# Performance work log

Hardware: AMD Instinct MI355X
Metric: run time of the kernel (lower is better)

Reference implementation:

```python
import jax, jax.numpy as jnp
import numpy as np

B, T, N, D, H = 8, 128, 64, 1024, 512

def setup_inputs() -> dict:
    key = jax.random.key(0)
    ks = jax.random.split(key, 8)
    s = 1.0 / np.sqrt(D)
    return {
        "img_features": jax.random.normal(ks[0], (B, T, N, D), dtype=jnp.float32),
        "hidden_state": jax.random.normal(ks[1], (N, B, D), dtype=jnp.float32),
        "W_weight": jax.random.normal(ks[2], (H, D), dtype=jnp.float32) * s,
        "W_bias": jax.random.normal(ks[3], (H,), dtype=jnp.float32) * s,
        "U_weight": jax.random.normal(ks[4], (H, D), dtype=jnp.float32) * s,
        "U_bias": jax.random.normal(ks[5], (H,), dtype=jnp.float32) * s,
        "w_weight": jax.random.normal(ks[6], (1, H), dtype=jnp.float32) * (1.0 / np.sqrt(H)),
        "w_bias": jax.random.normal(ks[7], (1,), dtype=jnp.float32) * (1.0 / np.sqrt(H)),
    }

def reference(img_features, hidden_state, W_weight, W_bias, U_weight, U_bias, w_weight, w_bias):
    # W_e: [B,T,N,H]
    W_e = jnp.einsum('btnd,hd->btnh', img_features, W_weight) + W_bias
    # U(hidden): [N,B,H]; torch unsqueeze(0).permute(2,0,1,3) -> [B,1,N,H]
    U_h = jnp.einsum('nbd,hd->nbh', hidden_state, U_weight) + U_bias
    U_e = jnp.transpose(U_h, (1, 0, 2))[:, None, :, :]  # [B,1,N,H]
    att = jnp.tanh(W_e + U_e)                            # [B,T,N,H]
    e = jnp.einsum('btnh,h->btn', att, w_weight[0]) + w_bias[0]  # [B,T,N]
    alpha = jax.nn.softmax(e, axis=-1)                   # softmax over objects N
    phi = jnp.einsum('btnd,btn->btd', img_features, alpha)  # [B,T,D]
    return phi
```

## Files before the change

kernel.cpp:

```cpp
#include <hip/hip_runtime.h>
#include <stdint.h>

#define B_ 8
#define T_ 128
#define N_ 64
#define D_ 1024
#define H_ 512

typedef __attribute__((ext_vector_type(8))) short bf16x8;
typedef __attribute__((ext_vector_type(4))) float f32x4;

__device__ __forceinline__ unsigned short f2bf(float x) {
  union { float f; unsigned u; } c; c.f = x;
  unsigned r = c.u + 0x7FFFu + ((c.u >> 16) & 1u);
  return (unsigned short)(r >> 16);
}

__global__ __launch_bounds__(256) void k_transU(const float* __restrict__ U,
                                                float* __restrict__ Ut) {
  __shared__ float tile[32][33];
  int d0 = blockIdx.x * 32, h0 = blockIdx.y * 32;
  int lx = threadIdx.x & 31, ly = threadIdx.x >> 5;
#pragma unroll
  for (int i = 0; i < 32; i += 8)
    tile[ly + i][lx] = U[(size_t)(h0 + ly + i) * D_ + d0 + lx];
  __syncthreads();
#pragma unroll
  for (int i = 0; i < 32; i += 8)
    Ut[(size_t)(d0 + ly + i) * H_ + h0 + lx] = tile[lx][ly + i];
}

__global__ __launch_bounds__(512) void k_convW(const float* __restrict__ W,
                                               unsigned short* __restrict__ Wt) {
  int i = blockIdx.x * 512 + threadIdx.x;
  int e = i & 7, cs = (i >> 3) & 3, h = (i >> 5) & 511, kt = i >> 14;
  int k = kt * 32 + (((cs ^ (h & 3)) << 3) | e);
  Wt[i] = f2bf(W[(size_t)h * D_ + k]);
}

__global__ __launch_bounds__(512) void k_uh(const float* __restrict__ hidden,
                                            const float* __restrict__ Ut,
                                            const float* __restrict__ Ub,
                                            const float* __restrict__ Wb,
                                            float* __restrict__ Uhb) {
  __shared__ float xs[8][1024];
  int b = blockIdx.x >> 3, ng = blockIdx.x & 7, tid = threadIdx.x;
  for (int i = tid; i < 8192; i += 512) {
    int nn = i >> 10, d = i & 1023;
    xs[nn][d] = hidden[(size_t)((ng * 8 + nn) * B_ + b) * D_ + d];
  }
  __syncthreads();
  float acc[8];
#pragma unroll
  for (int nn = 0; nn < 8; ++nn) acc[nn] = 0.f;
  for (int d = 0; d < 1024; ++d) {
    float u = Ut[(size_t)d * H_ + tid];
#pragma unroll
    for (int nn = 0; nn < 8; ++nn) acc[nn] += xs[nn][d] * u;
  }
  float bias = Ub[tid] + Wb[tid];
#pragma unroll
  for (int nn = 0; nn < 8; ++nn)
    Uhb[(size_t)(b * 64 + ng * 8 + nn) * H_ + tid] = acc[nn] + bias;
}

__global__ __launch_bounds__(512, 2) void k_main(const float* __restrict__ img,
                                                 const unsigned short* __restrict__ Wt,
                                                 const float* __restrict__ Uhb,
                                                 const float* __restrict__ ww,
                                                 const float* __restrict__ wb,
                                                 float* __restrict__ alpha) {
  __shared__ __align__(16) unsigned char sA[4096];
  __shared__ __align__(16) unsigned char sB[32768];
  __shared__ float e_part[256];
  const int tid = threadIdx.x;
  const int bt = blockIdx.x;
  const int b = bt >> 7;
  const int lane = tid & 63, w = tid >> 6, wm = w >> 2, wn = w & 3;
  const int lo = lane & 15, hi = lane >> 4;

  const int rowA = tid >> 3, c4 = tid & 7;
  const float* gA = img + (size_t)bt * 65536 + rowA * 1024 + c4 * 4;
  const int sAoff = rowA * 64 + ((((c4 >> 1) ^ (rowA & 3)) << 4) | ((c4 & 1) << 3));
  const uint4* gB = (const uint4*)Wt;

  const int swz = ((hi ^ (lane & 3)) << 4);
  const int base_a = (wm * 32 + lo) * 64 + swz;
  const int base_b = (wn * 128 + lo) * 64 + swz;

  f32x4 acc[2][8] = {};

  for (int kt = 0; kt < 32; ++kt) {
    float4 av = *(const float4*)(gA + kt * 32);
    uint4 b0 = gB[kt * 2048 + 0 * 512 + tid];
    uint4 b1 = gB[kt * 2048 + 1 * 512 + tid];
    uint4 b2 = gB[kt * 2048 + 2 * 512 + tid];
    uint4 b3 = gB[kt * 2048 + 3 * 512 + tid];
    uint2 pk;
    pk.x = (unsigned)f2bf(av.x) | ((unsigned)f2bf(av.y) << 16);
    pk.y = (unsigned)f2bf(av.z) | ((unsigned)f2bf(av.w) << 16);
    *(uint2*)(sA + sAoff) = pk;
    *(uint4*)(sB + (0 * 512 + tid) * 16) = b0;
    *(uint4*)(sB + (1 * 512 + tid) * 16) = b1;
    *(uint4*)(sB + (2 * 512 + tid) * 16) = b2;
    *(uint4*)(sB + (3 * 512 + tid) * 16) = b3;
    __syncthreads();

    bf16x8 aF0 = *(const bf16x8*)(sA + base_a);
    bf16x8 aF1 = *(const bf16x8*)(sA + base_a + 1024);
    bf16x8 bF[8];
#pragma unroll
    for (int nf = 0; nf < 8; ++nf) bF[nf] = *(const bf16x8*)(sB + base_b + nf * 1024);
#pragma unroll
    for (int nf = 0; nf < 8; ++nf) {
      acc[0][nf] = __builtin_amdgcn_mfma_f32_16x16x32_bf16(aF0, bF[nf], acc[0][nf], 0, 0, 0);
      acc[1][nf] = __builtin_amdgcn_mfma_f32_16x16x32_bf16(aF1, bF[nf], acc[1][nf], 0, 0, 0);
    }
    __syncthreads();
  }

  float ep[2][4] = {{0.f, 0.f, 0.f, 0.f}, {0.f, 0.f, 0.f, 0.f}};
  const float* Ubase = Uhb + (size_t)b * 64 * 512;
#pragma unroll
  for (int mf = 0; mf < 2; ++mf) {
#pragma unroll
    for (int r = 0; r < 4; ++r) {
      const int row = wm * 32 + mf * 16 + hi * 4 + r;
      const float* urow = Ubase + (size_t)row * 512;
      float s = 0.f;
#pragma unroll
      for (int nf = 0; nf < 8; ++nf) {
        const int h = wn * 128 + nf * 16 + lo;
        float v = acc[mf][nf][r] + urow[h];
        s += tanhf(v) * ww[h];
      }
      ep[mf][r] = s;
    }
  }
#pragma unroll
  for (int mf = 0; mf < 2; ++mf) {
#pragma unroll
    for (int r = 0; r < 4; ++r) {
      float v = ep[mf][r];
      v += __shfl_xor(v, 1);
      v += __shfl_xor(v, 2);
      v += __shfl_xor(v, 4);
      v += __shfl_xor(v, 8);
      if (lo == 0) e_part[(wm * 32 + mf * 16 + hi * 4 + r) * 4 + wn] = v;
    }
  }
  __syncthreads();
  if (tid < 64) {
    float e = e_part[tid * 4] + e_part[tid * 4 + 1] + e_part[tid * 4 + 2] +
              e_part[tid * 4 + 3] + wb[0];
    float m = e;
#pragma unroll
    for (int s = 32; s; s >>= 1) m = fmaxf(m, __shfl_xor(m, s));
    float p = expf(e - m);
    float su = p;
#pragma unroll
    for (int s = 32; s; s >>= 1) su += __shfl_xor(su, s);
    alpha[bt * 64 + tid] = p / su;
  }
}

__global__ __launch_bounds__(256) void k_phi(const float* __restrict__ img,
                                             const float* __restrict__ alpha,
                                             float* __restrict__ out) {
  __shared__ float alf[64];
  int bt = blockIdx.x, tid = threadIdx.x;
  if (tid < 64) alf[tid] = alpha[bt * 64 + tid];
  __syncthreads();
  const float4* ip = (const float4*)img + (size_t)bt * 16384 + tid;
  float4 s = make_float4(0.f, 0.f, 0.f, 0.f);
#pragma unroll 8
  for (int n = 0; n < 64; ++n) {
    float a = alf[n];
    float4 v = ip[(size_t)n * 256];
    s.x += a * v.x; s.y += a * v.y; s.z += a * v.z; s.w += a * v.w;
  }
  ((float4*)out)[(size_t)bt * 256 + tid] = s;
}

extern "C" void kernel_launch(void* const* d_in, const int* in_sizes, int n_in,
                              void* d_out, int out_size, void* d_ws, size_t ws_size,
                              hipStream_t stream) {
  const float* img    = (const float*)d_in[0];
  const float* hidden = (const float*)d_in[1];
  const float* Ww     = (const float*)d_in[2];
  const float* Wb     = (const float*)d_in[3];
  const float* Uw     = (const float*)d_in[4];
  const float* Ub     = (const float*)d_in[5];
  const float* ww     = (const float*)d_in[6];
  const float* wb     = (const float*)d_in[7];
  float* out = (float*)d_out;
  char* ws = (char*)d_ws;

  float* Ut            = (float*)ws;
  unsigned short* Wt   = (unsigned short*)(ws + (2u << 20));
  float* Uhb           = (float*)(ws + (3u << 20));
  float* alpha         = (float*)ws;

  k_transU<<<dim3(32, 16), 256, 0, stream>>>(Uw, Ut);
  k_convW<<<1024, 512, 0, stream>>>(Ww, Wt);
  k_uh<<<64, 512, 0, stream>>>(hidden, Ut, Ub, Wb, Uhb);
  k_main<<<1024, 512, 0, stream>>>(img, Wt, Uhb, ww, wb, alpha);
  k_phi<<<1024, 256, 0, stream>>>(img, alpha, out);
}
```

Baseline: 719.6 us.

## Double-buffer LDS tiles in main GEMM and batch U loads in k_uh

k_main now uses two LDS buffers: global loads for the next K tile are issued before the MFMAs on the current tile and stored to the alternate buffer afterwards, leaving one barrier per iteration. This hides global load latency behind matrix math. Launch bounds are raised to 4 blocks per CU, which tightens the register budget and may force spills while LDS doubling limits real occupancy. k_uh batches eight Ut loads per step to expose more memory parallelism.

```diff
diff --git a/kernel.cpp b/kernel.cpp
--- a/kernel.cpp
+++ b/kernel.cpp
@@ -53,10 +53,15 @@
   float acc[8];
 #pragma unroll
   for (int nn = 0; nn < 8; ++nn) acc[nn] = 0.f;
-  for (int d = 0; d < 1024; ++d) {
-    float u = Ut[(size_t)d * H_ + tid];
-#pragma unroll
-    for (int nn = 0; nn < 8; ++nn) acc[nn] += xs[nn][d] * u;
+  for (int d0 = 0; d0 < 1024; d0 += 8) {
+    float u[8];
+#pragma unroll
+    for (int j = 0; j < 8; ++j) u[j] = Ut[(size_t)(d0 + j) * H_ + tid];
+#pragma unroll
+    for (int j = 0; j < 8; ++j) {
+#pragma unroll
+      for (int nn = 0; nn < 8; ++nn) acc[nn] += xs[nn][d0 + j] * u[j];
+    }
   }
   float bias = Ub[tid] + Wb[tid];
 #pragma unroll
@@ -64,14 +69,14 @@
     Uhb[(size_t)(b * 64 + ng * 8 + nn) * H_ + tid] = acc[nn] + bias;
 }
 
-__global__ __launch_bounds__(512, 2) void k_main(const float* __restrict__ img,
+__global__ __launch_bounds__(512, 4) void k_main(const float* __restrict__ img,
                                                  const unsigned short* __restrict__ Wt,
                                                  const float* __restrict__ Uhb,
                                                  const float* __restrict__ ww,
                                                  const float* __restrict__ wb,
                                                  float* __restrict__ alpha) {
-  __shared__ __align__(16) unsigned char sA[4096];
-  __shared__ __align__(16) unsigned char sB[32768];
+  __shared__ __align__(16) unsigned char sA[2][4096];
+  __shared__ __align__(16) unsigned char sB[2][32768];
   __shared__ float e_part[256];
   const int tid = threadIdx.x;
   const int bt = blockIdx.x;
@@ -90,31 +95,79 @@
 
   f32x4 acc[2][8] = {};
 
-  for (int kt = 0; kt < 32; ++kt) {
-    float4 av = *(const float4*)(gA + kt * 32);
-    uint4 b0 = gB[kt * 2048 + 0 * 512 + tid];
-    uint4 b1 = gB[kt * 2048 + 1 * 512 + tid];
-    uint4 b2 = gB[kt * 2048 + 2 * 512 + tid];
-    uint4 b3 = gB[kt * 2048 + 3 * 512 + tid];
+  {
+    float4 av = *(const float4*)(gA);
+    uint4 b0 = gB[0 * 512 + tid];
+    uint4 b1 = gB[1 * 512 + tid];
+    uint4 b2 = gB[2 * 512 + tid];
+    uint4 b3 = gB[3 * 512 + tid];
     uint2 pk;
     pk.x = (unsigned)f2bf(av.x) | ((unsigned)f2bf(av.y) << 16);
     pk.y = (unsigned)f2bf(av.z) | ((unsigned)f2bf(av.w) << 16);
-    *(uint2*)(sA + sAoff) = pk;
-    *(uint4*)(sB + (0 * 512 + tid) * 16) = b0;
-    *(uint4*)(sB + (1 * 512 + tid) * 16) = b1;
-    *(uint4*)(sB + (2 * 512 + tid) * 16) = b2;
-    *(uint4*)(sB + (3 * 512 + tid) * 16) = b3;
-    __syncthreads();
-
-    bf16x8 aF0 = *(const bf16x8*)(sA + base_a);
-    bf16x8 aF1 = *(const bf16x8*)(sA + base_a + 1024);
-    bf16x8 bF[8];
-#pragma unroll
-    for (int nf = 0; nf < 8; ++nf) bF[nf] = *(const bf16x8*)(sB + base_b + nf * 1024);
-#pragma unroll
-    for (int nf = 0; nf < 8; ++nf) {
-      acc[0][nf] = __builtin_amdgcn_mfma_f32_16x16x32_bf16(aF0, bF[nf], acc[0][nf], 0, 0, 0);
-      acc[1][nf] = __builtin_amdgcn_mfma_f32_16x16x32_bf16(aF1, bF[nf], acc[1][nf], 0, 0, 0);
+    *(uint2*)(sA[0] + sAoff) = pk;
+    *(uint4*)(sB[0] + (0 * 512 + tid) * 16) = b0;
+    *(uint4*)(sB[0] + (1 * 512 + tid) * 16) = b1;
+    *(uint4*)(sB[0] + (2 * 512 + tid) * 16) = b2;
+    *(uint4*)(sB[0] + (3 * 512 + tid) * 16) = b3;
+  }
+  __syncthreads();
+
+  for (int kt = 0; kt < 32; ++kt) {
+    const int cur = kt & 1;
+    float4 av;
+    uint4 nb0, nb1, nb2, nb3;
+    if (kt < 31) {
+      av = *(const float4*)(gA + (kt + 1) * 32);
+      const uint4* gBk = gB + (size_t)(kt + 1) * 2048;
+      nb0 = gBk[0 * 512 + tid];
+      nb1 = gBk[1 * 512 + tid];
+      nb2 = gBk[2 * 512 + tid];
+      nb3 = gBk[3 * 512 + tid];
+    }
+
+    const unsigned char* cA = sA[cur];
+    const unsigned char* cB = sB[cur];
+    bf16x8 aF0 = *(const bf16x8*)(cA + base_a);
+    bf16x8 aF1 = *(const bf16x8*)(cA + base_a + 1024);
+    {
+      bf16x8 bF0 = *(const bf16x8*)(cB + base_b + 0 * 1024);
+      bf16x8 bF1 = *(const bf16x8*)(cB + base_b + 1 * 1024);
+      bf16x8 bF2 = *(const bf16x8*)(cB + base_b + 2 * 1024);
+      bf16x8 bF3 = *(const bf16x8*)(cB + base_b + 3 * 1024);
+      acc[0][0] = __builtin_amdgcn_mfma_f32_16x16x32_bf16(aF0, bF0, acc[0][0], 0, 0, 0);
+      acc[1][0] = __builtin_amdgcn_mfma_f32_16x16x32_bf16(aF1, bF0, acc[1][0], 0, 0, 0);
+      acc[0][1] = __builtin_amdgcn_mfma_f32_16x16x32_bf16(aF0, bF1, acc[0][1], 0, 0, 0);
+      acc[1][1] = __builtin_amdgcn_mfma_f32_16x16x32_bf16(aF1, bF1, acc[1][1], 0, 0, 0);
+      acc[0][2] = __builtin_amdgcn_mfma_f32_16x16x32_bf16(aF0, bF2, acc[0][2], 0, 0, 0);
+      acc[1][2] = __builtin_amdgcn_mfma_f32_16x16x32_bf16(aF1, bF2, acc[1][2], 0, 0, 0);
+      acc[0][3] = __builtin_amdgcn_mfma_f32_16x16x32_bf16(aF0, bF3, acc[0][3], 0, 0, 0);
+      acc[1][3] = __builtin_amdgcn_mfma_f32_16x16x32_bf16(aF1, bF3, acc[1][3], 0, 0, 0);
+    }
+    {
+      bf16x8 bF4 = *(const bf16x8*)(cB + base_b + 4 * 1024);
+      bf16x8 bF5 = *(const bf16x8*)(cB + base_b + 5 * 1024);
+      bf16x8 bF6 = *(const bf16x8*)(cB + base_b + 6 * 1024);
+      bf16x8 bF7 = *(const bf16x8*)(cB + base_b + 7 * 1024);
+      acc[0][4] = __builtin_amdgcn_mfma_f32_16x16x32_bf16(aF0, bF4, acc[0][4], 0, 0, 0);
+      acc[1][4] = __builtin_amdgcn_mfma_f32_16x16x32_bf16(aF1, bF4, acc[1][4], 0, 0, 0);
+      acc[0][5] = __builtin_amdgcn_mfma_f32_16x16x32_bf16(aF0, bF5, acc[0][5], 0, 0, 0);
+      acc[1][5] = __builtin_amdgcn_mfma_f32_16x16x32_bf16(aF1, bF5, acc[1][5], 0, 0, 0);
+      acc[0][6] = __builtin_amdgcn_mfma_f32_16x16x32_bf16(aF0, bF6, acc[0][6], 0, 0, 0);
+      acc[1][6] = __builtin_amdgcn_mfma_f32_16x16x32_bf16(aF1, bF6, acc[1][6], 0, 0, 0);
+      acc[0][7] = __builtin_amdgcn_mfma_f32_16x16x32_bf16(aF0, bF7, acc[0][7], 0, 0, 0);
+      acc[1][7] = __builtin_amdgcn_mfma_f32_16x16x32_bf16(aF1, bF7, acc[1][7], 0, 0, 0);
+    }
+
+    if (kt < 31) {
+      const int nxt = cur ^ 1;
+      uint2 pk;
+      pk.x = (unsigned)f2bf(av.x) | ((unsigned)f2bf(av.y) << 16);
+      pk.y = (unsigned)f2bf(av.z) | ((unsigned)f2bf(av.w) << 16);
+      *(uint2*)(sA[nxt] + sAoff) = pk;
+      *(uint4*)(sB[nxt] + (0 * 512 + tid) * 16) = nb0;
+      *(uint4*)(sB[nxt] + (1 * 512 + tid) * 16) = nb1;
+      *(uint4*)(sB[nxt] + (2 * 512 + tid) * 16) = nb2;
+      *(uint4*)(sB[nxt] + (3 * 512 + tid) * 16) = nb3;
     }
     __syncthreads();
   }
```

Result: faster. 598.3 us (-16.8%).
